# Kernel tuning notes

Measured on AMD Instinct MI355X. Metric: run time of the kernel, lower is better.

## Reference

```python
import jax, jax.numpy as jnp
import numpy as np

B, T, DIN, DOUT = 64, 512, 512, 512


def setup_inputs() -> dict:
    key = jax.random.key(0)
    ks = jax.random.split(key, 8)
    s_in = 1.0 / np.sqrt(DIN)
    s_h = 1.0 / np.sqrt(DOUT)
    return {
        "X": jax.random.normal(ks[0], (B, T, DIN), dtype=jnp.float32),
        "mask": jnp.ones((B, T), dtype=jnp.int32),
        "W_z": jax.random.normal(ks[1], (DIN, DOUT), dtype=jnp.float32) * s_in,
        "U_z": jax.random.normal(ks[2], (DOUT, DOUT), dtype=jnp.float32) * s_h,
        "b_z": jnp.zeros((DOUT,), dtype=jnp.float32),
        "W_r": jax.random.normal(ks[3], (DIN, DOUT), dtype=jnp.float32) * s_in,
        "U_r": jax.random.normal(ks[4], (DOUT, DOUT), dtype=jnp.float32) * s_h,
        "b_r": jnp.zeros((DOUT,), dtype=jnp.float32),
        "W_h": jax.random.normal(ks[5], (DIN, DOUT), dtype=jnp.float32) * s_in,
        "U_h": jax.random.normal(ks[6], (DOUT, DOUT), dtype=jnp.float32) * s_h,
        "b_h": jnp.zeros((DOUT,), dtype=jnp.float32),
    }


def reference(X, mask, W_z, U_z, b_z, W_r, U_r, b_r, W_h, U_h, b_h):
    # Precompute input projections for all timesteps (as the original does),
    # then scan the recurrence over time. return_sequences=False -> final h.
    # time-major: [T, B, DOUT]
    x_z = jnp.einsum('btd,dh->tbh', X, W_z) + b_z
    x_r = jnp.einsum('btd,dh->tbh', X, W_r) + b_r
    x_h = jnp.einsum('btd,dh->tbh', X, W_h) + b_h
    m = mask.T[:, :, None]  # [T, B, 1]

    def step(h, inp):
        xz_t, xr_t, xh_t, m_t = inp
        z = jax.nn.sigmoid(xz_t + h @ U_z)
        r = jax.nn.sigmoid(xr_t + h @ U_r)
        hh = jnp.tanh(xh_t + (r * h) @ U_h)
        h_new = z * h + (1.0 - z) * hh
        h_new = jnp.where(m_t > 0, h_new, h)  # masked steps keep previous state
        return h_new, None

    h0 = jnp.zeros((X.shape[0], U_z.shape[0]), dtype=X.dtype)
    h_final, _ = jax.lax.scan(step, h0, (x_z, x_r, x_h, m))
    return h_final
```

## Files before the change

### kernel.cpp

```cpp
#include <hip/hip_runtime.h>
#include <stdint.h>


#define GT    512
#define GDIN  512
#define GDOUT 512
#define NGRP  8
#define NSL   16
#define GROWS 8
#define COLS  32
#define NWAVE 8
#define KW    64
#define NWG   (NGRP * NSL)

#define OFF_HB    0
#define OFF_RHB   (2 * NGRP * GROWS * GDOUT)
#define OFF_HFL   (OFF_RHB + NGRP * GROWS * GDOUT)
#define FLSTR     4
#define FLGRP     (NSL * NWAVE * FLSTR)
#define OFF_RFL   (OFF_HFL + NGRP * FLGRP)
#define OFF_CNS   (OFF_RFL + NGRP * FLGRP)
#define CNS_DW    160
#define INIT_DW   (OFF_CNS + CNS_DW)

typedef __attribute__((ext_vector_type(8))) short bf16x8;
typedef __attribute__((ext_vector_type(4))) float f32x4;
typedef __attribute__((ext_vector_type(4))) unsigned int u32x4;

__device__ __forceinline__ short f2bf(float f) {
  union { float f; uint32_t u; } v; v.f = f;
  uint32_t r = (v.u + 0x7FFFu + ((v.u >> 16) & 1u)) >> 16;
  return (short)(uint16_t)r;
}
__device__ __forceinline__ float bf2f(short s) {
  union { uint32_t u; float f; } v; v.u = ((uint32_t)(uint16_t)s) << 16;
  return v.f;
}
__device__ __forceinline__ uint32_t pack_hl(float v) {
  short hi = f2bf(v);
  short lo = f2bf(v - bf2f(hi));
  return ((uint32_t)(uint16_t)hi << 16) | (uint32_t)(uint16_t)lo;
}

__device__ __forceinline__ void st_sc1(uint32_t* p, uint32_t v) {
  asm volatile("global_store_dword %0, %1, off sc1" :: "v"(p), "v"(v) : "memory");
}
__device__ __forceinline__ void st_pl(uint32_t* p, uint32_t v) {
  asm volatile("global_store_dword %0, %1, off" :: "v"(p), "v"(v) : "memory");
}
__device__ __forceinline__ void vm_drain() {
  asm volatile("s_waitcnt vmcnt(0)" ::: "memory");
}
__device__ __forceinline__ void l1_inv() {
  asm volatile("buffer_inv sc1" ::: "memory");
}
__device__ __forceinline__ uint32_t ld_nt(const uint32_t* p) {
  uint32_t v;
  asm volatile("global_load_dword %0, %1, off nt\n\ts_waitcnt vmcnt(0)"
               : "=v"(v) : "v"(p) : "memory");
  return v;
}

__device__ __forceinline__ void slab4_sc1(const uint32_t* base, u32x4 d[4]) {
  asm volatile(
    "global_load_dwordx4 %0, %4, off sc1\n\t"
    "global_load_dwordx4 %1, %4, off offset:16 sc1\n\t"
    "global_load_dwordx4 %2, %4, off offset:128 sc1\n\t"
    "global_load_dwordx4 %3, %4, off offset:144 sc1\n\t"
    "s_waitcnt vmcnt(0)"
    : "=&v"(d[0]), "=&v"(d[1]), "=&v"(d[2]), "=&v"(d[3])
    : "v"(base) : "memory");
}
__device__ __forceinline__ void slab4_nt(const uint32_t* base, u32x4 d[4]) {
  asm volatile(
    "global_load_dwordx4 %0, %4, off nt\n\t"
    "global_load_dwordx4 %1, %4, off offset:16 nt\n\t"
    "global_load_dwordx4 %2, %4, off offset:128 nt\n\t"
    "global_load_dwordx4 %3, %4, off offset:144 nt\n\t"
    "s_waitcnt vmcnt(0)"
    : "=&v"(d[0]), "=&v"(d[1]), "=&v"(d[2]), "=&v"(d[3])
    : "v"(base) : "memory");
}

__device__ __forceinline__ void wait16(const uint32_t* fbase, uint32_t tgt,
                                       int lane, int wv, int fast, int& budget) {
  if (budget <= 0) return;
  const int idx = lane & 15;
  const uint32_t* p = fbase +
      (size_t)(((2 * wv + (idx >> 3)) * NWAVE + (idx & 7)) * FLSTR);
  if (fast) {
    for (;;) {
      uint32_t v = ld_nt(p);
      if (__all((int)(v >= tgt))) break;
      if (--budget <= 0) break;
    }
  } else {
    for (;;) {
      uint32_t v = __hip_atomic_load(p, __ATOMIC_RELAXED, __HIP_MEMORY_SCOPE_AGENT);
      if (__all((int)(v >= tgt))) break;
      if (--budget <= 0) break;
    }
  }
  asm volatile("" ::: "memory");
}

union U16x8 { uint32_t u[4]; bf16x8 v; };
__device__ __forceinline__ void mk_frags(const u32x4 A, const u32x4 B,
                                         bf16x8& hi, bf16x8& lo) {
  U16x8 h, l;
  h.u[0] = (A[0] >> 16) | (A[1] & 0xFFFF0000u);  l.u[0] = (A[0] & 0xFFFFu) | (A[1] << 16);
  h.u[1] = (A[2] >> 16) | (A[3] & 0xFFFF0000u);  l.u[1] = (A[2] & 0xFFFFu) | (A[3] << 16);
  h.u[2] = (B[0] >> 16) | (B[1] & 0xFFFF0000u);  l.u[2] = (B[0] & 0xFFFFu) | (B[1] << 16);
  h.u[3] = (B[2] >> 16) | (B[3] & 0xFFFF0000u);  l.u[3] = (B[2] & 0xFFFFu) | (B[3] << 16);
  hi = h.v; lo = l.v;
}

__global__ __launch_bounds__(512, 2)
void gru_fused(const float* __restrict__ X, const int* __restrict__ mask,
               const float* __restrict__ Wz, const float* __restrict__ Uz,
               const float* __restrict__ bz,
               const float* __restrict__ Wr, const float* __restrict__ Ur,
               const float* __restrict__ br,
               const float* __restrict__ Wh, const float* __restrict__ Uh,
               const float* __restrict__ bh,
               float* __restrict__ out, uint32_t* __restrict__ ws)
{
  const int tid   = threadIdx.x;
  const int wv    = tid >> 6;
  const int lane  = tid & 63;
  const int col16 = lane & 15;
  const int quad  = lane >> 4;
  const int row8  = lane & 7;

  uint32_t* cns = ws + OFF_CNS;
  __shared__ int s_mode, s_g, s_sl;
  if (tid == 0) {
    uint32_t xcc = 0;
    asm volatile("s_getreg_b32 %0, hwreg(HW_REG_XCC_ID)" : "=s"(xcc));
    xcc &= 7u;
    uint32_t slot = __hip_atomic_fetch_add(&cns[xcc], 1u, __ATOMIC_RELAXED,
                                           __HIP_MEMORY_SCOPE_AGENT);
    if (slot >= (uint32_t)NSL)
      __hip_atomic_fetch_add(&cns[9], 1u, __ATOMIC_RELAXED, __HIP_MEMORY_SCOPE_AGENT);
    __hip_atomic_fetch_add(&cns[8], 1u, __ATOMIC_RELEASE, __HIP_MEMORY_SCOPE_AGENT);
    uint32_t tv = 0; long sp = 0;
    do {
      tv = __hip_atomic_load(&cns[8], __ATOMIC_ACQUIRE, __HIP_MEMORY_SCOPE_AGENT);
    } while (tv < (uint32_t)NWG && ++sp < 2000000L);
    uint32_t bad = __hip_atomic_load(&cns[9], __ATOMIC_RELAXED, __HIP_MEMORY_SCOPE_AGENT);
    const int cok = (tv >= (uint32_t)NWG && bad == 0u);
    int g_, sl_, mode_ = 0;
    if (cok) {
      g_ = (int)xcc; sl_ = (int)slot;
      l1_inv();
      uint32_t* tok = cns + 16;
      st_pl(&tok[g_ * NSL + sl_], 1u);
      vm_drain();
      const uint32_t* np = &tok[g_ * NSL + ((sl_ + 1) & (NSL - 1))];
      int ok = 0;
      for (long i = 0; i < 300000L; ++i) {
        if (ld_nt(np) != 0u) { ok = 1; break; }
      }
      if (!ok)
        __hip_atomic_fetch_add(&cns[11], 1u, __ATOMIC_RELAXED, __HIP_MEMORY_SCOPE_AGENT);
      __hip_atomic_fetch_add(&cns[10], 1u, __ATOMIC_RELEASE, __HIP_MEMORY_SCOPE_AGENT);
      uint32_t tv2 = 0; sp = 0;
      do {
        tv2 = __hip_atomic_load(&cns[10], __ATOMIC_ACQUIRE, __HIP_MEMORY_SCOPE_AGENT);
      } while (tv2 < (uint32_t)NWG && ++sp < 2000000L);
      uint32_t fl = __hip_atomic_load(&cns[11], __ATOMIC_RELAXED, __HIP_MEMORY_SCOPE_AGENT);
      mode_ = (tv2 >= (uint32_t)NWG && fl == 0u) ? 1 : 0;
    } else {
      g_ = (int)(blockIdx.x & 7); sl_ = (int)(blockIdx.x >> 3);
    }
    s_mode = mode_; s_g = g_; s_sl = sl_;
  }
  __syncthreads();
  const int fast = __builtin_amdgcn_readfirstlane(s_mode);
  const int g    = __builtin_amdgcn_readfirstlane(s_g);
  const int sl   = __builtin_amdgcn_readfirstlane(s_sl);
  l1_inv();

  const int jb = sl * COLS;
  const int kb = wv * KW;

  uint32_t* hb  = ws + OFF_HB;
  uint32_t* rhb = ws + OFF_RHB;
  uint32_t* hfl = ws + OFF_HFL + (size_t)g * FLGRP;
  uint32_t* rfl = ws + OFF_RFL + (size_t)g * FLGRP;
  uint32_t* hfl_my = hfl + (size_t)(sl * NWAVE + wv) * FLSTR;
  uint32_t* rfl_my = rfl + (size_t)(sl * NWAVE + wv) * FLSTR;
  uint32_t* rhg = rhb + (size_t)g * (GROWS * GDOUT);
  const int slab_off = row8 * GDOUT + kb + quad * 8;

  __shared__ __align__(16) float scrA[2][NWAVE][2][GROWS][COLS];
  __shared__ __align__(16) float scrB[2][NWAVE][GROWS][COLS];

  bf16x8 uzh[2][2], uzl[2][2], urh[2][2], url[2][2], uhh[2][2], uhl[2][2];
  bf16x8 wzf[2][2], wrf[2][2], whf[2][2];
#pragma unroll
  for (int c = 0; c < 2; ++c) {
#pragma unroll
    for (int Tt = 0; Tt < 2; ++Tt) {
      const int k0 = kb + c * 32 + quad * 8;
      const int j  = jb + Tt * 16 + col16;
      bf16x8 t_uzh, t_uzl, t_urh, t_url, t_uhh, t_uhl, t_wz, t_wr, t_wh;
#pragma unroll
      for (int i = 0; i < 8; ++i) {
        const int idx = (k0 + i) * GDOUT + j;
        float u; short hi;
        u = Uz[idx]; hi = f2bf(u); t_uzh[i] = hi; t_uzl[i] = f2bf(u - bf2f(hi));
        u = Ur[idx]; hi = f2bf(u); t_urh[i] = hi; t_url[i] = f2bf(u - bf2f(hi));
        u = Uh[idx]; hi = f2bf(u); t_uhh[i] = hi; t_uhl[i] = f2bf(u - bf2f(hi));
        t_wz[i] = f2bf(Wz[idx]);
        t_wr[i] = f2bf(Wr[idx]);
        t_wh[i] = f2bf(Wh[idx]);
      }
      uzh[c][Tt] = t_uzh; uzl[c][Tt] = t_uzl; urh[c][Tt] = t_urh; url[c][Tt] = t_url;
      uhh[c][Tt] = t_uhh; uhl[c][Tt] = t_uhl;
      wzf[c][Tt] = t_wz;  wrf[c][Tt] = t_wr;  whf[c][Tt] = t_wh;
    }
  }

  const int ecol = lane & 31;
  const float bzv = bz[jb + ecol];
  const float brv = br[jb + ecol];
  const float bhv = bh[jb + ecol];
  const int b_ep = GROWS * g + wv;

  float hreg = 0.f;
  float zvl  = 0.f;
  int budget = 4000000;

  for (int t = 0; t < GT; ++t) {
    const int par = t & 1;
    bf16x8 xa[2];
#pragma unroll
    for (int c = 0; c < 2; ++c) {
      const int k0 = kb + c * 32 + quad * 8;
      const float* xp = X + ((size_t)(GROWS * g + row8) * GT + t) * GDIN + k0;
      f32x4 x0 = *(const f32x4*)xp;
      f32x4 x1 = *(const f32x4*)(xp + 4);
      bf16x8 xf;
#pragma unroll
      for (int i = 0; i < 4; ++i) { xf[i] = f2bf(x0[i]); xf[i + 4] = f2bf(x1[i]); }
      xa[c] = xf;
    }
    const int mk = mask[(size_t)b_ep * GT + t];

    if (t) wait16(hfl, (uint32_t)t, lane, wv, fast, budget);
    const uint32_t* hsrc = hb + ((size_t)par * NGRP + g) * (GROWS * GDOUT) + slab_off;
    u32x4 hd[4];
    if (fast) slab4_nt(hsrc, hd); else slab4_sc1(hsrc, hd);

    f32x4 az[2]  = {{0,0,0,0},{0,0,0,0}}, az2[2] = {{0,0,0,0},{0,0,0,0}};
    f32x4 ar[2]  = {{0,0,0,0},{0,0,0,0}}, ar2[2] = {{0,0,0,0},{0,0,0,0}};
    f32x4 ah[2]  = {{0,0,0,0},{0,0,0,0}};
#pragma unroll
    for (int c = 0; c < 2; ++c) {
      bf16x8 hhi, hlo;
      mk_frags(hd[2 * c], hd[2 * c + 1], hhi, hlo);
#pragma unroll
      for (int Tt = 0; Tt < 2; ++Tt) {
        az[Tt]  = __builtin_amdgcn_mfma_f32_16x16x32_bf16(hhi, uzh[c][Tt], az[Tt],  0, 0, 0);
        az2[Tt] = __builtin_amdgcn_mfma_f32_16x16x32_bf16(hlo, uzh[c][Tt], az2[Tt], 0, 0, 0);
        az[Tt]  = __builtin_amdgcn_mfma_f32_16x16x32_bf16(hhi, uzl[c][Tt], az[Tt],  0, 0, 0);
        az2[Tt] = __builtin_amdgcn_mfma_f32_16x16x32_bf16(xa[c], wzf[c][Tt], az2[Tt], 0, 0, 0);
        ar[Tt]  = __builtin_amdgcn_mfma_f32_16x16x32_bf16(hhi, urh[c][Tt], ar[Tt],  0, 0, 0);
        ar2[Tt] = __builtin_amdgcn_mfma_f32_16x16x32_bf16(hlo, urh[c][Tt], ar2[Tt], 0, 0, 0);
        ar[Tt]  = __builtin_amdgcn_mfma_f32_16x16x32_bf16(hhi, url[c][Tt], ar[Tt],  0, 0, 0);
        ar2[Tt] = __builtin_amdgcn_mfma_f32_16x16x32_bf16(xa[c], wrf[c][Tt], ar2[Tt], 0, 0, 0);
        ah[Tt]  = __builtin_amdgcn_mfma_f32_16x16x32_bf16(xa[c], whf[c][Tt], ah[Tt],  0, 0, 0);
      }
    }

    if (quad < 2) {
#pragma unroll
      for (int Tt = 0; Tt < 2; ++Tt)
#pragma unroll
        for (int rr = 0; rr < 4; ++rr) {
          scrA[par][wv][0][quad * 4 + rr][Tt * 16 + col16] = az[Tt][rr] + az2[Tt][rr];
          scrA[par][wv][1][quad * 4 + rr][Tt * 16 + col16] = ar[Tt][rr] + ar2[Tt][rr];
        }
    }
    __syncthreads();

    float zsum = 0.f, rsum = 0.f;
#pragma unroll
    for (int w2 = 0; w2 < NWAVE; ++w2) {
      zsum += scrA[par][w2][0][wv][ecol];
      rsum += scrA[par][w2][1][wv][ecol];
    }
    zvl = 1.f / (1.f + __expf(-(zsum + bzv)));
    const float rvl = 1.f / (1.f + __expf(-(rsum + brv)));
    if (lane < 32) {
      uint32_t* dst = rhg + (size_t)wv * GDOUT + jb + lane;
      const uint32_t pv = pack_hl(rvl * hreg);
      if (fast) st_pl(dst, pv); else st_sc1(dst, pv);
    }
    vm_drain();
    if (lane == 0) {
      if (fast) st_pl(rfl_my, (uint32_t)(t + 1)); else st_sc1(rfl_my, (uint32_t)(t + 1));
    }

    wait16(rfl, (uint32_t)(t + 1), lane, wv, fast, budget);
    u32x4 rd[4];
    const uint32_t* rsrc = rhg + slab_off;
    if (fast) slab4_nt(rsrc, rd); else slab4_sc1(rsrc, rd);

    f32x4 b1[2] = {{0,0,0,0},{0,0,0,0}}, b2[2] = {{0,0,0,0},{0,0,0,0}};
    f32x4 b3[2] = {{0,0,0,0},{0,0,0,0}};
#pragma unroll
    for (int c = 0; c < 2; ++c) {
      bf16x8 th, tl;
      mk_frags(rd[2 * c], rd[2 * c + 1], th, tl);
#pragma unroll
      for (int Tt = 0; Tt < 2; ++Tt) {
        b1[Tt] = __builtin_amdgcn_mfma_f32_16x16x32_bf16(th, uhh[c][Tt], b1[Tt], 0, 0, 0);
        b2[Tt] = __builtin_amdgcn_mfma_f32_16x16x32_bf16(tl, uhh[c][Tt], b2[Tt], 0, 0, 0);
        b3[Tt] = __builtin_amdgcn_mfma_f32_16x16x32_bf16(th, uhl[c][Tt], b3[Tt], 0, 0, 0);
      }
    }

    if (quad < 2) {
#pragma unroll
      for (int Tt = 0; Tt < 2; ++Tt)
#pragma unroll
        for (int rr = 0; rr < 4; ++rr)
          scrB[par][wv][quad * 4 + rr][Tt * 16 + col16] =
              ah[Tt][rr] + b1[Tt][rr] + b2[Tt][rr] + b3[Tt][rr];
    }
    __syncthreads();

    float hsum = 0.f;
#pragma unroll
    for (int w2 = 0; w2 < NWAVE; ++w2) hsum += scrB[par][w2][wv][ecol];
    const float pre = hsum + bhv;
    const float e  = __expf(2.f * pre);
    const float hh = 1.f - 2.f / (e + 1.f);
    float hn = zvl * hreg + (1.f - zvl) * hh;
    hn = (mk > 0) ? hn : hreg;
    hreg = hn;

    if (lane < 32) {
      uint32_t* hdst = hb + ((size_t)((t + 1) & 1) * NGRP + g) * (GROWS * GDOUT)
                         + (size_t)wv * GDOUT + jb + lane;
      const uint32_t pv = pack_hl(hn);
      if (fast) st_pl(hdst, pv); else st_sc1(hdst, pv);
      if (t == GT - 1) out[(size_t)b_ep * GDOUT + jb + lane] = hn;
    }
    vm_drain();
    if (lane == 0) {
      if (fast) st_pl(hfl_my, (uint32_t)(t + 1)); else st_sc1(hfl_my, (uint32_t)(t + 1));
    }
  }
}

extern "C" void kernel_launch(void* const* d_in, const int* in_sizes, int n_in,
                              void* d_out, int out_size, void* d_ws, size_t ws_size,
                              hipStream_t stream) {
  const float* X  = (const float*)d_in[0];
  const int* mask = (const int*)d_in[1];
  const float* Wz = (const float*)d_in[2];
  const float* Uz = (const float*)d_in[3];
  const float* bz = (const float*)d_in[4];
  const float* Wr = (const float*)d_in[5];
  const float* Ur = (const float*)d_in[6];
  const float* br = (const float*)d_in[7];
  const float* Wh = (const float*)d_in[8];
  const float* Uh = (const float*)d_in[9];
  const float* bh = (const float*)d_in[10];

  hipMemsetAsync(d_ws, 0, (size_t)INIT_DW * 4, stream);

  hipLaunchKernelGGL(gru_fused, dim3(NWG), dim3(512), 0, stream,
                     X, mask, Wz, Uz, bz, Wr, Ur, br, Wh, Uh, bh,
                     (float*)d_out, (uint32_t*)d_ws);
}
```

Measured before the change: 2.643 ms.

## Tag each hidden-state word with its timestep to replace separate flag barriers

Adds a tagged-payload path in which every hidden-state and r*h value is stored together with its timestep tag using one 64-bit store. Consumers spin directly on the data slab until every tag matches, which removes the separate flag store, the vmcnt drain and the flag polling from the inter-workgroup handshake. The change also prefetches the next step's X and mask while waiting and moves the W_h input MFMAs to run during the r-exchange wait. In exchange the slab reads are doubled in size, and the path is selected only when the workspace is large enough; otherwise the old flag-based loop (with the same prefetch changes) runs.

```diff
diff --git a/kernel.cpp b/kernel.cpp
--- a/kernel.cpp
+++ b/kernel.cpp
@@ -13,19 +13,27 @@
 #define KW    64
 #define NWG   (NGRP * NSL)
 
-#define OFF_HB    0
-#define OFF_RHB   (2 * NGRP * GROWS * GDOUT)
-#define OFF_HFL   (OFF_RHB + NGRP * GROWS * GDOUT)
-#define FLSTR     4
-#define FLGRP     (NSL * NWAVE * FLSTR)
-#define OFF_RFL   (OFF_HFL + NGRP * FLGRP)
-#define OFF_CNS   (OFF_RFL + NGRP * FLGRP)
-#define CNS_DW    160
-#define INIT_DW   (OFF_CNS + CNS_DW)
+#define FLSTR 4
+#define FLGRP (NSL * NWAVE * FLSTR)
+
+#define T_OFF_HB   0
+#define T_OFF_RHB  (NGRP * GROWS * 1024)
+#define T_OFF_HFL  (T_OFF_RHB + NGRP * GROWS * 1024)
+#define T_OFF_RFL  (T_OFF_HFL + NGRP * FLGRP)
+#define T_OFF_CNS  (T_OFF_RFL + NGRP * FLGRP)
+#define T_INIT_DW  (T_OFF_CNS + 160)
+
+#define C_OFF_HB   0
+#define C_OFF_RHB  (2 * NGRP * GROWS * 512)
+#define C_OFF_HFL  (C_OFF_RHB + NGRP * GROWS * 512)
+#define C_OFF_RFL  (C_OFF_HFL + NGRP * FLGRP)
+#define C_OFF_CNS  (C_OFF_RFL + NGRP * FLGRP)
+#define C_INIT_DW  (C_OFF_CNS + 160)
 
 typedef __attribute__((ext_vector_type(8))) short bf16x8;
 typedef __attribute__((ext_vector_type(4))) float f32x4;
 typedef __attribute__((ext_vector_type(4))) unsigned int u32x4;
+typedef __attribute__((ext_vector_type(2))) unsigned int u32x2;
 
 __device__ __forceinline__ short f2bf(float f) {
   union { float f; uint32_t u; } v; v.f = f;
@@ -47,6 +55,13 @@
 }
 __device__ __forceinline__ void st_pl(uint32_t* p, uint32_t v) {
   asm volatile("global_store_dword %0, %1, off" :: "v"(p), "v"(v) : "memory");
+}
+__device__ __forceinline__ void st2(uint32_t* p, uint32_t pay, uint32_t tag, int fast) {
+  u32x2 v; v[0] = pay; v[1] = tag;
+  if (fast)
+    asm volatile("global_store_dwordx2 %0, %1, off" :: "v"(p), "v"(v) : "memory");
+  else
+    asm volatile("global_store_dwordx2 %0, %1, off sc1" :: "v"(p), "v"(v) : "memory");
 }
 __device__ __forceinline__ void vm_drain() {
   asm volatile("s_waitcnt vmcnt(0)" ::: "memory");
@@ -59,6 +74,52 @@
   asm volatile("global_load_dword %0, %1, off nt\n\ts_waitcnt vmcnt(0)"
                : "=v"(v) : "v"(p) : "memory");
   return v;
+}
+
+__device__ __forceinline__ void slab8p(const uint32_t* base, u32x4 d[8], int fast) {
+  if (fast) {
+    asm volatile(
+      "global_load_dwordx4 %0, %8, off nt\n\t"
+      "global_load_dwordx4 %1, %8, off offset:16 nt\n\t"
+      "global_load_dwordx4 %2, %8, off offset:32 nt\n\t"
+      "global_load_dwordx4 %3, %8, off offset:48 nt\n\t"
+      "global_load_dwordx4 %4, %8, off offset:256 nt\n\t"
+      "global_load_dwordx4 %5, %8, off offset:272 nt\n\t"
+      "global_load_dwordx4 %6, %8, off offset:288 nt\n\t"
+      "global_load_dwordx4 %7, %8, off offset:304 nt\n\t"
+      "s_waitcnt vmcnt(0)"
+      : "=&v"(d[0]), "=&v"(d[1]), "=&v"(d[2]), "=&v"(d[3]),
+        "=&v"(d[4]), "=&v"(d[5]), "=&v"(d[6]), "=&v"(d[7])
+      : "v"(base) : "memory");
+  } else {
+    asm volatile(
+      "global_load_dwordx4 %0, %8, off sc1\n\t"
+      "global_load_dwordx4 %1, %8, off offset:16 sc1\n\t"
+      "global_load_dwordx4 %2, %8, off offset:32 sc1\n\t"
+      "global_load_dwordx4 %3, %8, off offset:48 sc1\n\t"
+      "global_load_dwordx4 %4, %8, off offset:256 sc1\n\t"
+      "global_load_dwordx4 %5, %8, off offset:272 sc1\n\t"
+      "global_load_dwordx4 %6, %8, off offset:288 sc1\n\t"
+      "global_load_dwordx4 %7, %8, off offset:304 sc1\n\t"
+      "s_waitcnt vmcnt(0)"
+      : "=&v"(d[0]), "=&v"(d[1]), "=&v"(d[2]), "=&v"(d[3]),
+        "=&v"(d[4]), "=&v"(d[5]), "=&v"(d[6]), "=&v"(d[7])
+      : "v"(base) : "memory");
+  }
+}
+__device__ __forceinline__ void slabp_wait(const uint32_t* base, uint32_t tgt,
+                                           u32x4 d[8], int check, int fast,
+                                           int& budget) {
+  for (;;) {
+    slab8p(base, d, fast);
+    if (!check) return;
+    uint32_t x = (d[0][1]^tgt)|(d[0][3]^tgt)|(d[1][1]^tgt)|(d[1][3]^tgt)
+               | (d[2][1]^tgt)|(d[2][3]^tgt)|(d[3][1]^tgt)|(d[3][3]^tgt)
+               | (d[4][1]^tgt)|(d[4][3]^tgt)|(d[5][1]^tgt)|(d[5][3]^tgt)
+               | (d[6][1]^tgt)|(d[6][3]^tgt)|(d[7][1]^tgt)|(d[7][3]^tgt);
+    if (__all((int)(x == 0u))) return;
+    if (--budget <= 0) return;
+  }
 }
 
 __device__ __forceinline__ void slab4_sc1(const uint32_t* base, u32x4 d[4]) {
@@ -81,7 +142,6 @@
     : "=&v"(d[0]), "=&v"(d[1]), "=&v"(d[2]), "=&v"(d[3])
     : "v"(base) : "memory");
 }
-
 __device__ __forceinline__ void wait16(const uint32_t* fbase, uint32_t tgt,
                                        int lane, int wv, int fast, int& budget) {
   if (budget <= 0) return;
@@ -123,7 +183,7 @@
                const float* __restrict__ br,
                const float* __restrict__ Wh, const float* __restrict__ Uh,
                const float* __restrict__ bh,
-               float* __restrict__ out, uint32_t* __restrict__ ws)
+               float* __restrict__ out, uint32_t* __restrict__ ws, int tagL)
 {
   const int tid   = threadIdx.x;
   const int wv    = tid >> 6;
@@ -132,7 +192,7 @@
   const int quad  = lane >> 4;
   const int row8  = lane & 7;
 
-  uint32_t* cns = ws + OFF_CNS;
+  uint32_t* cns = ws + (tagL ? T_OFF_CNS : C_OFF_CNS);
   __shared__ int s_mode, s_g, s_sl;
   if (tid == 0) {
     uint32_t xcc = 0;
@@ -184,15 +244,6 @@
   const int jb = sl * COLS;
   const int kb = wv * KW;
 
-  uint32_t* hb  = ws + OFF_HB;
-  uint32_t* rhb = ws + OFF_RHB;
-  uint32_t* hfl = ws + OFF_HFL + (size_t)g * FLGRP;
-  uint32_t* rfl = ws + OFF_RFL + (size_t)g * FLGRP;
-  uint32_t* hfl_my = hfl + (size_t)(sl * NWAVE + wv) * FLSTR;
-  uint32_t* rfl_my = rfl + (size_t)(sl * NWAVE + wv) * FLSTR;
-  uint32_t* rhg = rhb + (size_t)g * (GROWS * GDOUT);
-  const int slab_off = row8 * GDOUT + kb + quad * 8;
-
   __shared__ __align__(16) float scrA[2][NWAVE][2][GROWS][COLS];
   __shared__ __align__(16) float scrB[2][NWAVE][GROWS][COLS];
 
@@ -232,126 +283,290 @@
   float zvl  = 0.f;
   int budget = 4000000;
 
-  for (int t = 0; t < GT; ++t) {
-    const int par = t & 1;
-    bf16x8 xa[2];
+  f32x4 xpA[2], xpB[2]; int mkpre;
+  {
+    const float* xr = X + (size_t)(GROWS * g + row8) * GT * GDIN;
 #pragma unroll
     for (int c = 0; c < 2; ++c) {
-      const int k0 = kb + c * 32 + quad * 8;
-      const float* xp = X + ((size_t)(GROWS * g + row8) * GT + t) * GDIN + k0;
-      f32x4 x0 = *(const f32x4*)xp;
-      f32x4 x1 = *(const f32x4*)(xp + 4);
-      bf16x8 xf;
-#pragma unroll
-      for (int i = 0; i < 4; ++i) { xf[i] = f2bf(x0[i]); xf[i + 4] = f2bf(x1[i]); }
-      xa[c] = xf;
-    }
-    const int mk = mask[(size_t)b_ep * GT + t];
-
-    if (t) wait16(hfl, (uint32_t)t, lane, wv, fast, budget);
-    const uint32_t* hsrc = hb + ((size_t)par * NGRP + g) * (GROWS * GDOUT) + slab_off;
-    u32x4 hd[4];
-    if (fast) slab4_nt(hsrc, hd); else slab4_sc1(hsrc, hd);
-
-    f32x4 az[2]  = {{0,0,0,0},{0,0,0,0}}, az2[2] = {{0,0,0,0},{0,0,0,0}};
-    f32x4 ar[2]  = {{0,0,0,0},{0,0,0,0}}, ar2[2] = {{0,0,0,0},{0,0,0,0}};
-    f32x4 ah[2]  = {{0,0,0,0},{0,0,0,0}};
-#pragma unroll
-    for (int c = 0; c < 2; ++c) {
-      bf16x8 hhi, hlo;
-      mk_frags(hd[2 * c], hd[2 * c + 1], hhi, hlo);
-#pragma unroll
-      for (int Tt = 0; Tt < 2; ++Tt) {
-        az[Tt]  = __builtin_amdgcn_mfma_f32_16x16x32_bf16(hhi, uzh[c][Tt], az[Tt],  0, 0, 0);
-        az2[Tt] = __builtin_amdgcn_mfma_f32_16x16x32_bf16(hlo, uzh[c][Tt], az2[Tt], 0, 0, 0);
-        az[Tt]  = __builtin_amdgcn_mfma_f32_16x16x32_bf16(hhi, uzl[c][Tt], az[Tt],  0, 0, 0);
-        az2[Tt] = __builtin_amdgcn_mfma_f32_16x16x32_bf16(xa[c], wzf[c][Tt], az2[Tt], 0, 0, 0);
-        ar[Tt]  = __builtin_amdgcn_mfma_f32_16x16x32_bf16(hhi, urh[c][Tt], ar[Tt],  0, 0, 0);
-        ar2[Tt] = __builtin_amdgcn_mfma_f32_16x16x32_bf16(hlo, urh[c][Tt], ar2[Tt], 0, 0, 0);
-        ar[Tt]  = __builtin_amdgcn_mfma_f32_16x16x32_bf16(hhi, url[c][Tt], ar[Tt],  0, 0, 0);
-        ar2[Tt] = __builtin_amdgcn_mfma_f32_16x16x32_bf16(xa[c], wrf[c][Tt], ar2[Tt], 0, 0, 0);
-        ah[Tt]  = __builtin_amdgcn_mfma_f32_16x16x32_bf16(xa[c], whf[c][Tt], ah[Tt],  0, 0, 0);
-      }
-    }
-
-    if (quad < 2) {
-#pragma unroll
-      for (int Tt = 0; Tt < 2; ++Tt)
-#pragma unroll
-        for (int rr = 0; rr < 4; ++rr) {
-          scrA[par][wv][0][quad * 4 + rr][Tt * 16 + col16] = az[Tt][rr] + az2[Tt][rr];
-          scrA[par][wv][1][quad * 4 + rr][Tt * 16 + col16] = ar[Tt][rr] + ar2[Tt][rr];
+      const float* xp = xr + (size_t)0 * GDIN + kb + c * 32 + quad * 8;
+      xpA[c] = *(const f32x4*)xp;
+      xpB[c] = *(const f32x4*)(xp + 4);
+    }
+    mkpre = mask[(size_t)b_ep * GT + 0];
+  }
+
+  if (tagL) {
+    uint32_t* hbg = ws + T_OFF_HB  + (size_t)g * GROWS * 1024;
+    uint32_t* rhg = ws + T_OFF_RHB + (size_t)g * GROWS * 1024;
+    const int slab2 = row8 * 1024 + 2 * (kb + quad * 8);
+
+    for (int t = 0; t < GT; ++t) {
+      const int par = t & 1;
+      bf16x8 xa[2];
+#pragma unroll
+      for (int c = 0; c < 2; ++c) {
+        bf16x8 xf;
+#pragma unroll
+        for (int i = 0; i < 4; ++i) { xf[i] = f2bf(xpA[c][i]); xf[i + 4] = f2bf(xpB[c][i]); }
+        xa[c] = xf;
+      }
+      const int mk = mkpre;
+
+      u32x4 hd[8];
+      slabp_wait(hbg + slab2, (uint32_t)t, hd, t != 0, fast, budget);
+
+      f32x4 az[2]  = {{0,0,0,0},{0,0,0,0}}, az2[2] = {{0,0,0,0},{0,0,0,0}};
+      f32x4 ar[2]  = {{0,0,0,0},{0,0,0,0}}, ar2[2] = {{0,0,0,0},{0,0,0,0}};
+#pragma unroll
+      for (int c = 0; c < 2; ++c) {
+        u32x4 A; A[0]=hd[4*c][0]; A[1]=hd[4*c][2]; A[2]=hd[4*c+1][0]; A[3]=hd[4*c+1][2];
+        u32x4 B; B[0]=hd[4*c+2][0]; B[1]=hd[4*c+2][2]; B[2]=hd[4*c+3][0]; B[3]=hd[4*c+3][2];
+        bf16x8 hhi, hlo;
+        mk_frags(A, B, hhi, hlo);
+#pragma unroll
+        for (int Tt = 0; Tt < 2; ++Tt) {
+          az[Tt]  = __builtin_amdgcn_mfma_f32_16x16x32_bf16(hhi, uzh[c][Tt], az[Tt],  0, 0, 0);
+          az2[Tt] = __builtin_amdgcn_mfma_f32_16x16x32_bf16(hlo, uzh[c][Tt], az2[Tt], 0, 0, 0);
+          az[Tt]  = __builtin_amdgcn_mfma_f32_16x16x32_bf16(hhi, uzl[c][Tt], az[Tt],  0, 0, 0);
+          az2[Tt] = __builtin_amdgcn_mfma_f32_16x16x32_bf16(xa[c], wzf[c][Tt], az2[Tt], 0, 0, 0);
+          ar[Tt]  = __builtin_amdgcn_mfma_f32_16x16x32_bf16(hhi, urh[c][Tt], ar[Tt],  0, 0, 0);
+          ar2[Tt] = __builtin_amdgcn_mfma_f32_16x16x32_bf16(hlo, urh[c][Tt], ar2[Tt], 0, 0, 0);
+          ar[Tt]  = __builtin_amdgcn_mfma_f32_16x16x32_bf16(hhi, url[c][Tt], ar[Tt],  0, 0, 0);
+          ar2[Tt] = __builtin_amdgcn_mfma_f32_16x16x32_bf16(xa[c], wrf[c][Tt], ar2[Tt], 0, 0, 0);
         }
-    }
-    __syncthreads();
-
-    float zsum = 0.f, rsum = 0.f;
-#pragma unroll
-    for (int w2 = 0; w2 < NWAVE; ++w2) {
-      zsum += scrA[par][w2][0][wv][ecol];
-      rsum += scrA[par][w2][1][wv][ecol];
-    }
-    zvl = 1.f / (1.f + __expf(-(zsum + bzv)));
-    const float rvl = 1.f / (1.f + __expf(-(rsum + brv)));
-    if (lane < 32) {
-      uint32_t* dst = rhg + (size_t)wv * GDOUT + jb + lane;
-      const uint32_t pv = pack_hl(rvl * hreg);
-      if (fast) st_pl(dst, pv); else st_sc1(dst, pv);
-    }
-    vm_drain();
-    if (lane == 0) {
-      if (fast) st_pl(rfl_my, (uint32_t)(t + 1)); else st_sc1(rfl_my, (uint32_t)(t + 1));
-    }
-
-    wait16(rfl, (uint32_t)(t + 1), lane, wv, fast, budget);
-    u32x4 rd[4];
-    const uint32_t* rsrc = rhg + slab_off;
-    if (fast) slab4_nt(rsrc, rd); else slab4_sc1(rsrc, rd);
-
-    f32x4 b1[2] = {{0,0,0,0},{0,0,0,0}}, b2[2] = {{0,0,0,0},{0,0,0,0}};
-    f32x4 b3[2] = {{0,0,0,0},{0,0,0,0}};
-#pragma unroll
-    for (int c = 0; c < 2; ++c) {
-      bf16x8 th, tl;
-      mk_frags(rd[2 * c], rd[2 * c + 1], th, tl);
-#pragma unroll
-      for (int Tt = 0; Tt < 2; ++Tt) {
-        b1[Tt] = __builtin_amdgcn_mfma_f32_16x16x32_bf16(th, uhh[c][Tt], b1[Tt], 0, 0, 0);
-        b2[Tt] = __builtin_amdgcn_mfma_f32_16x16x32_bf16(tl, uhh[c][Tt], b2[Tt], 0, 0, 0);
-        b3[Tt] = __builtin_amdgcn_mfma_f32_16x16x32_bf16(th, uhl[c][Tt], b3[Tt], 0, 0, 0);
-      }
-    }
-
-    if (quad < 2) {
-#pragma unroll
-      for (int Tt = 0; Tt < 2; ++Tt)
-#pragma unroll
-        for (int rr = 0; rr < 4; ++rr)
-          scrB[par][wv][quad * 4 + rr][Tt * 16 + col16] =
-              ah[Tt][rr] + b1[Tt][rr] + b2[Tt][rr] + b3[Tt][rr];
-    }
-    __syncthreads();
-
-    float hsum = 0.f;
-#pragma unroll
-    for (int w2 = 0; w2 < NWAVE; ++w2) hsum += scrB[par][w2][wv][ecol];
-    const float pre = hsum + bhv;
-    const float e  = __expf(2.f * pre);
-    const float hh = 1.f - 2.f / (e + 1.f);
-    float hn = zvl * hreg + (1.f - zvl) * hh;
-    hn = (mk > 0) ? hn : hreg;
-    hreg = hn;
-
-    if (lane < 32) {
-      uint32_t* hdst = hb + ((size_t)((t + 1) & 1) * NGRP + g) * (GROWS * GDOUT)
-                         + (size_t)wv * GDOUT + jb + lane;
-      const uint32_t pv = pack_hl(hn);
-      if (fast) st_pl(hdst, pv); else st_sc1(hdst, pv);
-      if (t == GT - 1) out[(size_t)b_ep * GDOUT + jb + lane] = hn;
-    }
-    vm_drain();
-    if (lane == 0) {
-      if (fast) st_pl(hfl_my, (uint32_t)(t + 1)); else st_sc1(hfl_my, (uint32_t)(t + 1));
+      }
+
+      if (quad < 2) {
+#pragma unroll
+        for (int Tt = 0; Tt < 2; ++Tt)
+#pragma unroll
+          for (int rr = 0; rr < 4; ++rr) {
+            scrA[par][wv][0][quad * 4 + rr][Tt * 16 + col16] = az[Tt][rr] + az2[Tt][rr];
+            scrA[par][wv][1][quad * 4 + rr][Tt * 16 + col16] = ar[Tt][rr] + ar2[Tt][rr];
+          }
+      }
+      __syncthreads();
+
+      float zsum = 0.f, rsum = 0.f;
+#pragma unroll
+      for (int w2 = 0; w2 < NWAVE; ++w2) {
+        zsum += scrA[par][w2][0][wv][ecol];
+        rsum += scrA[par][w2][1][wv][ecol];
+      }
+      zvl = 1.f / (1.f + __expf(-(zsum + bzv)));
+      const float rvl = 1.f / (1.f + __expf(-(rsum + brv)));
+      if (lane < 32)
+        st2(rhg + (size_t)wv * 1024 + (size_t)(jb + lane) * 2,
+            pack_hl(rvl * hreg), (uint32_t)(t + 1), fast);
+
+      f32x4 ah[2] = {{0,0,0,0},{0,0,0,0}};
+#pragma unroll
+      for (int c = 0; c < 2; ++c)
+#pragma unroll
+        for (int Tt = 0; Tt < 2; ++Tt)
+          ah[Tt] = __builtin_amdgcn_mfma_f32_16x16x32_bf16(xa[c], whf[c][Tt], ah[Tt], 0, 0, 0);
+
+      u32x4 rd[8];
+      slabp_wait(rhg + slab2, (uint32_t)(t + 1), rd, 1, fast, budget);
+
+      {
+        const int tn = (t + 1 < GT) ? t + 1 : t;
+        const float* xr = X + (size_t)(GROWS * g + row8) * GT * GDIN;
+#pragma unroll
+        for (int c = 0; c < 2; ++c) {
+          const float* xp = xr + (size_t)tn * GDIN + kb + c * 32 + quad * 8;
+          xpA[c] = *(const f32x4*)xp;
+          xpB[c] = *(const f32x4*)(xp + 4);
+        }
+        mkpre = mask[(size_t)b_ep * GT + tn];
+      }
+
+      f32x4 b1[2] = {{0,0,0,0},{0,0,0,0}}, b2[2] = {{0,0,0,0},{0,0,0,0}};
+      f32x4 b3[2] = {{0,0,0,0},{0,0,0,0}};
+#pragma unroll
+      for (int c = 0; c < 2; ++c) {
+        u32x4 A; A[0]=rd[4*c][0]; A[1]=rd[4*c][2]; A[2]=rd[4*c+1][0]; A[3]=rd[4*c+1][2];
+        u32x4 B; B[0]=rd[4*c+2][0]; B[1]=rd[4*c+2][2]; B[2]=rd[4*c+3][0]; B[3]=rd[4*c+3][2];
+        bf16x8 th, tl;
+        mk_frags(A, B, th, tl);
+#pragma unroll
+        for (int Tt = 0; Tt < 2; ++Tt) {
+          b1[Tt] = __builtin_amdgcn_mfma_f32_16x16x32_bf16(th, uhh[c][Tt], b1[Tt], 0, 0, 0);
+          b2[Tt] = __builtin_amdgcn_mfma_f32_16x16x32_bf16(tl, uhh[c][Tt], b2[Tt], 0, 0, 0);
+          b3[Tt] = __builtin_amdgcn_mfma_f32_16x16x32_bf16(th, uhl[c][Tt], b3[Tt], 0, 0, 0);
+        }
+      }
+
+      if (quad < 2) {
+#pragma unroll
+        for (int Tt = 0; Tt < 2; ++Tt)
+#pragma unroll
+          for (int rr = 0; rr < 4; ++rr)
+            scrB[par][wv][quad * 4 + rr][Tt * 16 + col16] =
+                ah[Tt][rr] + b1[Tt][rr] + b2[Tt][rr] + b3[Tt][rr];
+      }
+      __syncthreads();
+
+      float hsum = 0.f;
+#pragma unroll
+      for (int w2 = 0; w2 < NWAVE; ++w2) hsum += scrB[par][w2][wv][ecol];
+      const float pre = hsum + bhv;
+      const float e  = __expf(2.f * pre);
+      const float hh = 1.f - 2.f / (e + 1.f);
+      float hn = zvl * hreg + (1.f - zvl) * hh;
+      hn = (mk > 0) ? hn : hreg;
+      hreg = hn;
+
+      if (lane < 32) {
+        st2(hbg + (size_t)wv * 1024 + (size_t)(jb + lane) * 2,
+            pack_hl(hn), (uint32_t)(t + 1), fast);
+        if (t == GT - 1) out[(size_t)b_ep * GDOUT + jb + lane] = hn;
+      }
+    }
+  } else {
+    uint32_t* hb  = ws + C_OFF_HB;
+    uint32_t* rhb = ws + C_OFF_RHB;
+    uint32_t* hfl = ws + C_OFF_HFL + (size_t)g * FLGRP;
+    uint32_t* rfl = ws + C_OFF_RFL + (size_t)g * FLGRP;
+    uint32_t* hfl_my = hfl + (size_t)(sl * NWAVE + wv) * FLSTR;
+    uint32_t* rfl_my = rfl + (size_t)(sl * NWAVE + wv) * FLSTR;
+    uint32_t* rhg = rhb + (size_t)g * (GROWS * GDOUT);
+    const int slab_off = row8 * GDOUT + kb + quad * 8;
+
+    for (int t = 0; t < GT; ++t) {
+      const int par = t & 1;
+      bf16x8 xa[2];
+#pragma unroll
+      for (int c = 0; c < 2; ++c) {
+        bf16x8 xf;
+#pragma unroll
+        for (int i = 0; i < 4; ++i) { xf[i] = f2bf(xpA[c][i]); xf[i + 4] = f2bf(xpB[c][i]); }
+        xa[c] = xf;
+      }
+      const int mk = mkpre;
+
+      if (t) wait16(hfl, (uint32_t)t, lane, wv, fast, budget);
+      const uint32_t* hsrc = hb + ((size_t)par * NGRP + g) * (GROWS * GDOUT) + slab_off;
+      u32x4 hd[4];
+      if (fast) slab4_nt(hsrc, hd); else slab4_sc1(hsrc, hd);
+
+      f32x4 az[2]  = {{0,0,0,0},{0,0,0,0}}, az2[2] = {{0,0,0,0},{0,0,0,0}};
+      f32x4 ar[2]  = {{0,0,0,0},{0,0,0,0}}, ar2[2] = {{0,0,0,0},{0,0,0,0}};
+#pragma unroll
+      for (int c = 0; c < 2; ++c) {
+        bf16x8 hhi, hlo;
+        mk_frags(hd[2 * c], hd[2 * c + 1], hhi, hlo);
+#pragma unroll
+        for (int Tt = 0; Tt < 2; ++Tt) {
+          az[Tt]  = __builtin_amdgcn_mfma_f32_16x16x32_bf16(hhi, uzh[c][Tt], az[Tt],  0, 0, 0);
+          az2[Tt] = __builtin_amdgcn_mfma_f32_16x16x32_bf16(hlo, uzh[c][Tt], az2[Tt], 0, 0, 0);
+          az[Tt]  = __builtin_amdgcn_mfma_f32_16x16x32_bf16(hhi, uzl[c][Tt], az[Tt],  0, 0, 0);
+          az2[Tt] = __builtin_amdgcn_mfma_f32_16x16x32_bf16(xa[c], wzf[c][Tt], az2[Tt], 0, 0, 0);
+          ar[Tt]  = __builtin_amdgcn_mfma_f32_16x16x32_bf16(hhi, urh[c][Tt], ar[Tt],  0, 0, 0);
+          ar2[Tt] = __builtin_amdgcn_mfma_f32_16x16x32_bf16(hlo, urh[c][Tt], ar2[Tt], 0, 0, 0);
+          ar[Tt]  = __builtin_amdgcn_mfma_f32_16x16x32_bf16(hhi, url[c][Tt], ar[Tt],  0, 0, 0);
+          ar2[Tt] = __builtin_amdgcn_mfma_f32_16x16x32_bf16(xa[c], wrf[c][Tt], ar2[Tt], 0, 0, 0);
+        }
+      }
+
+      if (quad < 2) {
+#pragma unroll
+        for (int Tt = 0; Tt < 2; ++Tt)
+#pragma unroll
+          for (int rr = 0; rr < 4; ++rr) {
+            scrA[par][wv][0][quad * 4 + rr][Tt * 16 + col16] = az[Tt][rr] + az2[Tt][rr];
+            scrA[par][wv][1][quad * 4 + rr][Tt * 16 + col16] = ar[Tt][rr] + ar2[Tt][rr];
+          }
+      }
+      __syncthreads();
+
+      float zsum = 0.f, rsum = 0.f;
+#pragma unroll
+      for (int w2 = 0; w2 < NWAVE; ++w2) {
+        zsum += scrA[par][w2][0][wv][ecol];
+        rsum += scrA[par][w2][1][wv][ecol];
+      }
+      zvl = 1.f / (1.f + __expf(-(zsum + bzv)));
+      const float rvl = 1.f / (1.f + __expf(-(rsum + brv)));
+      if (lane < 32) {
+        uint32_t* dst = rhg + (size_t)wv * GDOUT + jb + lane;
+        const uint32_t pv = pack_hl(rvl * hreg);
+        if (fast) st_pl(dst, pv); else st_sc1(dst, pv);
+      }
+      vm_drain();
+      if (lane == 0) {
+        if (fast) st_pl(rfl_my, (uint32_t)(t + 1)); else st_sc1(rfl_my, (uint32_t)(t + 1));
+      }
+
+      f32x4 ah[2] = {{0,0,0,0},{0,0,0,0}};
+#pragma unroll
+      for (int c = 0; c < 2; ++c)
+#pragma unroll
+        for (int Tt = 0; Tt < 2; ++Tt)
+          ah[Tt] = __builtin_amdgcn_mfma_f32_16x16x32_bf16(xa[c], whf[c][Tt], ah[Tt], 0, 0, 0);
+
+      wait16(rfl, (uint32_t)(t + 1), lane, wv, fast, budget);
+      u32x4 rd[4];
+      const uint32_t* rsrc = rhg + slab_off;
+      if (fast) slab4_nt(rsrc, rd); else slab4_sc1(rsrc, rd);
+
+      {
+        const int tn = (t + 1 < GT) ? t + 1 : t;
+        const float* xr = X + (size_t)(GROWS * g + row8) * GT * GDIN;
+#pragma unroll
+        for (int c = 0; c < 2; ++c) {
+          const float* xp = xr + (size_t)tn * GDIN + kb + c * 32 + quad * 8;
+          xpA[c] = *(const f32x4*)xp;
+          xpB[c] = *(const f32x4*)(xp + 4);
+        }
+        mkpre = mask[(size_t)b_ep * GT + tn];
+      }
+
+      f32x4 b1[2] = {{0,0,0,0},{0,0,0,0}}, b2[2] = {{0,0,0,0},{0,0,0,0}};
+      f32x4 b3[2] = {{0,0,0,0},{0,0,0,0}};
+#pragma unroll
+      for (int c = 0; c < 2; ++c) {
+        bf16x8 th, tl;
+        mk_frags(rd[2 * c], rd[2 * c + 1], th, tl);
+#pragma unroll
+        for (int Tt = 0; Tt < 2; ++Tt) {
+          b1[Tt] = __builtin_amdgcn_mfma_f32_16x16x32_bf16(th, uhh[c][Tt], b1[Tt], 0, 0, 0);
+          b2[Tt] = __builtin_amdgcn_mfma_f32_16x16x32_bf16(tl, uhh[c][Tt], b2[Tt], 0, 0, 0);
+          b3[Tt] = __builtin_amdgcn_mfma_f32_16x16x32_bf16(th, uhl[c][Tt], b3[Tt], 0, 0, 0);
+        }
+      }
+
+      if (quad < 2) {
+#pragma unroll
+        for (int Tt = 0; Tt < 2; ++Tt)
+#pragma unroll
+          for (int rr = 0; rr < 4; ++rr)
+            scrB[par][wv][quad * 4 + rr][Tt * 16 + col16] =
+                ah[Tt][rr] + b1[Tt][rr] + b2[Tt][rr] + b3[Tt][rr];
+      }
+      __syncthreads();
+
+      float hsum = 0.f;
+#pragma unroll
+      for (int w2 = 0; w2 < NWAVE; ++w2) hsum += scrB[par][w2][wv][ecol];
+      const float pre = hsum + bhv;
+      const float e  = __expf(2.f * pre);
+      const float hh = 1.f - 2.f / (e + 1.f);
+      float hn = zvl * hreg + (1.f - zvl) * hh;
+      hn = (mk > 0) ? hn : hreg;
+      hreg = hn;
+
+      if (lane < 32) {
+        uint32_t* hdst = hb + ((size_t)((t + 1) & 1) * NGRP + g) * (GROWS * GDOUT)
+                           + (size_t)wv * GDOUT + jb + lane;
+        const uint32_t pv = pack_hl(hn);
+        if (fast) st_pl(hdst, pv); else st_sc1(hdst, pv);
+        if (t == GT - 1) out[(size_t)b_ep * GDOUT + jb + lane] = hn;
+      }
+      vm_drain();
+      if (lane == 0) {
+        if (fast) st_pl(hfl_my, (uint32_t)(t + 1)); else st_sc1(hfl_my, (uint32_t)(t + 1));
+      }
     }
   }
 }
@@ -371,9 +586,10 @@
   const float* Uh = (const float*)d_in[9];
   const float* bh = (const float*)d_in[10];
 
-  hipMemsetAsync(d_ws, 0, (size_t)INIT_DW * 4, stream);
+  const int tagL = (ws_size >= (size_t)T_INIT_DW * 4) ? 1 : 0;
+  hipMemsetAsync(d_ws, 0, (size_t)(tagL ? T_INIT_DW : C_INIT_DW) * 4, stream);
 
   hipLaunchKernelGGL(gru_fused, dim3(NWG), dim3(512), 0, stream,
                      X, mask, Wz, Uz, bz, Wr, Ur, br, Wh, Uh, bh,
-                     (float*)d_out, (uint32_t*)d_ws);
-}
+                     (float*)d_out, (uint32_t*)d_ws, tagL);
+}
```

Measured after the change: 3.616 ms. 1.37x slower.

## Prefetch next-step X, overlap input MFMAs with h loads, pipeline flag polling

Applied to the files above, without the earlier changes.

Moves the X and mask loads for step t+1 into step t so their latency hides behind the flag wait, and splits the slab loads into issue and wait so the input-projection MFMAs run while h is in flight. The x_h projection now runs before the r-flag wait. Flag polling keeps two loads in flight, and bf16 packing uses the hardware v_cvt_pk_bf16_f32 instruction. In exchange it needs more registers, and the double-buffered polling adds a redundant outstanding load per wait.

```diff
diff --git a/kernel.cpp b/kernel.cpp
--- a/kernel.cpp
+++ b/kernel.cpp
@@ -20,8 +20,7 @@
 #define FLGRP     (NSL * NWAVE * FLSTR)
 #define OFF_RFL   (OFF_HFL + NGRP * FLGRP)
 #define OFF_CNS   (OFF_RFL + NGRP * FLGRP)
-#define CNS_DW    160
-#define INIT_DW   (OFF_CNS + CNS_DW)
+#define INIT_DW   (OFF_CNS + 160)
 
 typedef __attribute__((ext_vector_type(8))) short bf16x8;
 typedef __attribute__((ext_vector_type(4))) float f32x4;
@@ -37,9 +36,12 @@
   return v.f;
 }
 __device__ __forceinline__ uint32_t pack_hl(float v) {
-  short hi = f2bf(v);
-  short lo = f2bf(v - bf2f(hi));
-  return ((uint32_t)(uint16_t)hi << 16) | (uint32_t)(uint16_t)lo;
+  uint32_t t, o;
+  asm("v_cvt_pk_bf16_f32 %0, %1, %1" : "=v"(t) : "v"(v));
+  union { uint32_t u; float f; } hf; hf.u = t << 16;
+  float d = v - hf.f;
+  asm("v_cvt_pk_bf16_f32 %0, %1, %2" : "=v"(o) : "v"(d), "v"(v));
+  return o;
 }
 
 __device__ __forceinline__ void st_sc1(uint32_t* p, uint32_t v) {
@@ -61,25 +63,29 @@
   return v;
 }
 
-__device__ __forceinline__ void slab4_sc1(const uint32_t* base, u32x4 d[4]) {
-  asm volatile(
-    "global_load_dwordx4 %0, %4, off sc1\n\t"
-    "global_load_dwordx4 %1, %4, off offset:16 sc1\n\t"
-    "global_load_dwordx4 %2, %4, off offset:128 sc1\n\t"
-    "global_load_dwordx4 %3, %4, off offset:144 sc1\n\t"
-    "s_waitcnt vmcnt(0)"
-    : "=&v"(d[0]), "=&v"(d[1]), "=&v"(d[2]), "=&v"(d[3])
-    : "v"(base) : "memory");
-}
-__device__ __forceinline__ void slab4_nt(const uint32_t* base, u32x4 d[4]) {
-  asm volatile(
-    "global_load_dwordx4 %0, %4, off nt\n\t"
-    "global_load_dwordx4 %1, %4, off offset:16 nt\n\t"
-    "global_load_dwordx4 %2, %4, off offset:128 nt\n\t"
-    "global_load_dwordx4 %3, %4, off offset:144 nt\n\t"
-    "s_waitcnt vmcnt(0)"
-    : "=&v"(d[0]), "=&v"(d[1]), "=&v"(d[2]), "=&v"(d[3])
-    : "v"(base) : "memory");
+__device__ __forceinline__ void slab4_issue(const uint32_t* base, u32x4 d[4],
+                                            int fast) {
+  if (fast) {
+    asm volatile(
+      "global_load_dwordx4 %0, %4, off nt\n\t"
+      "global_load_dwordx4 %1, %4, off offset:16 nt\n\t"
+      "global_load_dwordx4 %2, %4, off offset:128 nt\n\t"
+      "global_load_dwordx4 %3, %4, off offset:144 nt"
+      : "=&v"(d[0]), "=&v"(d[1]), "=&v"(d[2]), "=&v"(d[3])
+      : "v"(base) : "memory");
+  } else {
+    asm volatile(
+      "global_load_dwordx4 %0, %4, off sc1\n\t"
+      "global_load_dwordx4 %1, %4, off offset:16 sc1\n\t"
+      "global_load_dwordx4 %2, %4, off offset:128 sc1\n\t"
+      "global_load_dwordx4 %3, %4, off offset:144 sc1"
+      : "=&v"(d[0]), "=&v"(d[1]), "=&v"(d[2]), "=&v"(d[3])
+      : "v"(base) : "memory");
+  }
+}
+__device__ __forceinline__ void slab_wait() {
+  asm volatile("s_waitcnt vmcnt(0)" ::: "memory");
+  __builtin_amdgcn_sched_barrier(0);
 }
 
 __device__ __forceinline__ void wait16(const uint32_t* fbase, uint32_t tgt,
@@ -89,11 +95,20 @@
   const uint32_t* p = fbase +
       (size_t)(((2 * wv + (idx >> 3)) * NWAVE + (idx & 7)) * FLSTR);
   if (fast) {
+    uint32_t v0, v1;
+    asm volatile("global_load_dword %0, %1, off nt" : "=v"(v0) : "v"(p) : "memory");
     for (;;) {
-      uint32_t v = ld_nt(p);
-      if (__all((int)(v >= tgt))) break;
-      if (--budget <= 0) break;
-    }
+      asm volatile("global_load_dword %0, %1, off nt" : "=v"(v1) : "v"(p) : "memory");
+      asm volatile("s_waitcnt vmcnt(1)" ::: "memory");
+      __builtin_amdgcn_sched_barrier(0);
+      if (__all((int)(v0 >= tgt))) break;
+      asm volatile("global_load_dword %0, %1, off nt" : "=v"(v0) : "v"(p) : "memory");
+      asm volatile("s_waitcnt vmcnt(1)" ::: "memory");
+      __builtin_amdgcn_sched_barrier(0);
+      if (__all((int)(v1 >= tgt))) break;
+      if ((budget -= 2) <= 0) break;
+    }
+    asm volatile("s_waitcnt vmcnt(0)" ::: "memory");
   } else {
     for (;;) {
       uint32_t v = __hip_atomic_load(p, __ATOMIC_RELAXED, __HIP_MEMORY_SCOPE_AGENT);
@@ -113,6 +128,14 @@
   h.u[2] = (B[0] >> 16) | (B[1] & 0xFFFF0000u);  l.u[2] = (B[0] & 0xFFFFu) | (B[1] << 16);
   h.u[3] = (B[2] >> 16) | (B[3] & 0xFFFF0000u);  l.u[3] = (B[2] & 0xFFFFu) | (B[3] << 16);
   hi = h.v; lo = l.v;
+}
+__device__ __forceinline__ bf16x8 cvt8(const f32x4 a, const f32x4 b) {
+  U16x8 w;
+  asm("v_cvt_pk_bf16_f32 %0, %1, %2" : "=v"(w.u[0]) : "v"(a[0]), "v"(a[1]));
+  asm("v_cvt_pk_bf16_f32 %0, %1, %2" : "=v"(w.u[1]) : "v"(a[2]), "v"(a[3]));
+  asm("v_cvt_pk_bf16_f32 %0, %1, %2" : "=v"(w.u[2]) : "v"(b[0]), "v"(b[1]));
+  asm("v_cvt_pk_bf16_f32 %0, %1, %2" : "=v"(w.u[3]) : "v"(b[2]), "v"(b[3]));
+  return w.v;
 }
 
 __global__ __launch_bounds__(512, 2)
@@ -232,30 +255,41 @@
   float zvl  = 0.f;
   int budget = 4000000;
 
+  f32x4 xpA[2], xpB[2]; int mkpre;
+  {
+    const float* xr = X + (size_t)(GROWS * g + row8) * GT * GDIN;
+#pragma unroll
+    for (int c = 0; c < 2; ++c) {
+      const float* xp = xr + kb + c * 32 + quad * 8;
+      xpA[c] = *(const f32x4*)xp;
+      xpB[c] = *(const f32x4*)(xp + 4);
+    }
+    mkpre = mask[(size_t)b_ep * GT + 0];
+  }
+
   for (int t = 0; t < GT; ++t) {
     const int par = t & 1;
     bf16x8 xa[2];
 #pragma unroll
-    for (int c = 0; c < 2; ++c) {
-      const int k0 = kb + c * 32 + quad * 8;
-      const float* xp = X + ((size_t)(GROWS * g + row8) * GT + t) * GDIN + k0;
-      f32x4 x0 = *(const f32x4*)xp;
-      f32x4 x1 = *(const f32x4*)(xp + 4);
-      bf16x8 xf;
-#pragma unroll
-      for (int i = 0; i < 4; ++i) { xf[i] = f2bf(x0[i]); xf[i + 4] = f2bf(x1[i]); }
-      xa[c] = xf;
-    }
-    const int mk = mask[(size_t)b_ep * GT + t];
+    for (int c = 0; c < 2; ++c) xa[c] = cvt8(xpA[c], xpB[c]);
+    const int mk = mkpre;
 
     if (t) wait16(hfl, (uint32_t)t, lane, wv, fast, budget);
     const uint32_t* hsrc = hb + ((size_t)par * NGRP + g) * (GROWS * GDOUT) + slab_off;
     u32x4 hd[4];
-    if (fast) slab4_nt(hsrc, hd); else slab4_sc1(hsrc, hd);
+    slab4_issue(hsrc, hd, fast);
 
     f32x4 az[2]  = {{0,0,0,0},{0,0,0,0}}, az2[2] = {{0,0,0,0},{0,0,0,0}};
     f32x4 ar[2]  = {{0,0,0,0},{0,0,0,0}}, ar2[2] = {{0,0,0,0},{0,0,0,0}};
-    f32x4 ah[2]  = {{0,0,0,0},{0,0,0,0}};
+#pragma unroll
+    for (int c = 0; c < 2; ++c)
+#pragma unroll
+      for (int Tt = 0; Tt < 2; ++Tt) {
+        az2[Tt] = __builtin_amdgcn_mfma_f32_16x16x32_bf16(xa[c], wzf[c][Tt], az2[Tt], 0, 0, 0);
+        ar2[Tt] = __builtin_amdgcn_mfma_f32_16x16x32_bf16(xa[c], wrf[c][Tt], ar2[Tt], 0, 0, 0);
+      }
+    slab_wait();
+
 #pragma unroll
     for (int c = 0; c < 2; ++c) {
       bf16x8 hhi, hlo;
@@ -265,12 +299,9 @@
         az[Tt]  = __builtin_amdgcn_mfma_f32_16x16x32_bf16(hhi, uzh[c][Tt], az[Tt],  0, 0, 0);
         az2[Tt] = __builtin_amdgcn_mfma_f32_16x16x32_bf16(hlo, uzh[c][Tt], az2[Tt], 0, 0, 0);
         az[Tt]  = __builtin_amdgcn_mfma_f32_16x16x32_bf16(hhi, uzl[c][Tt], az[Tt],  0, 0, 0);
-        az2[Tt] = __builtin_amdgcn_mfma_f32_16x16x32_bf16(xa[c], wzf[c][Tt], az2[Tt], 0, 0, 0);
         ar[Tt]  = __builtin_amdgcn_mfma_f32_16x16x32_bf16(hhi, urh[c][Tt], ar[Tt],  0, 0, 0);
         ar2[Tt] = __builtin_amdgcn_mfma_f32_16x16x32_bf16(hlo, urh[c][Tt], ar2[Tt], 0, 0, 0);
         ar[Tt]  = __builtin_amdgcn_mfma_f32_16x16x32_bf16(hhi, url[c][Tt], ar[Tt],  0, 0, 0);
-        ar2[Tt] = __builtin_amdgcn_mfma_f32_16x16x32_bf16(xa[c], wrf[c][Tt], ar2[Tt], 0, 0, 0);
-        ah[Tt]  = __builtin_amdgcn_mfma_f32_16x16x32_bf16(xa[c], whf[c][Tt], ah[Tt],  0, 0, 0);
       }
     }
 
@@ -303,10 +334,28 @@
       if (fast) st_pl(rfl_my, (uint32_t)(t + 1)); else st_sc1(rfl_my, (uint32_t)(t + 1));
     }
 
+    {
+      const int tn = (t + 1 < GT) ? t + 1 : t;
+      const float* xr = X + ((size_t)(GROWS * g + row8) * GT + tn) * GDIN;
+#pragma unroll
+      for (int c = 0; c < 2; ++c) {
+        const float* xp = xr + kb + c * 32 + quad * 8;
+        xpA[c] = *(const f32x4*)xp;
+        xpB[c] = *(const f32x4*)(xp + 4);
+      }
+      mkpre = mask[(size_t)b_ep * GT + tn];
+    }
+    f32x4 ah[2] = {{0,0,0,0},{0,0,0,0}};
+#pragma unroll
+    for (int c = 0; c < 2; ++c)
+#pragma unroll
+      for (int Tt = 0; Tt < 2; ++Tt)
+        ah[Tt] = __builtin_amdgcn_mfma_f32_16x16x32_bf16(xa[c], whf[c][Tt], ah[Tt], 0, 0, 0);
+
     wait16(rfl, (uint32_t)(t + 1), lane, wv, fast, budget);
     u32x4 rd[4];
-    const uint32_t* rsrc = rhg + slab_off;
-    if (fast) slab4_nt(rsrc, rd); else slab4_sc1(rsrc, rd);
+    slab4_issue(rhg + slab_off, rd, fast);
+    slab_wait();
 
     f32x4 b1[2] = {{0,0,0,0},{0,0,0,0}}, b2[2] = {{0,0,0,0},{0,0,0,0}};
     f32x4 b3[2] = {{0,0,0,0},{0,0,0,0}};
```

New measurement: 2.715 ms. +2.7%, slower.
